# Kernel optimization log

Hardware: AMD Instinct MI355X
Metric: run time of the kernel (lower is better)

The kernel has to match this reference:

```python
import jax, jax.numpy as jnp
import numpy as np

B, L, D1, D2, N = 4, 2048, 1024, 1024, 4096

def setup_inputs() -> dict:
    key = jax.random.key(0)
    k1, k2, k3 = jax.random.split(key, 3)
    inputs = jax.random.normal(k1, (B, L, D1), dtype=jnp.float32)
    key_param_tokens = jax.random.normal(k2, (N, D1), dtype=jnp.float32) * 0.02
    value_param_tokens = jax.random.normal(k3, (N, D2), dtype=jnp.float32) * 0.02
    return {"inputs": inputs, "key_param_tokens": key_param_tokens, "value_param_tokens": value_param_tokens}

def reference(inputs, key_param_tokens, value_param_tokens):
    # scores: [B, L, N] = query @ key^T (scale_factor = 1, no mask, dropout_p = 0)
    attn_weight = jnp.einsum('bld,nd->bln', inputs, key_param_tokens)
    n = attn_weight.shape[-1]
    # 'l2_norm_gelu': L2-normalize over the param-token axis, rescale by sqrt(n), then exact GELU
    l2 = jnp.sqrt(jnp.sum(attn_weight * attn_weight, axis=-1, keepdims=True))
    normed = attn_weight / l2 * jnp.sqrt(jnp.asarray(n, attn_weight.dtype))
    attn_weight = jax.nn.gelu(normed, approximate=False)
    # output: [B, L, D2]
    return jnp.einsum('bln,nd->bld', attn_weight, value_param_tokens)
```

## Files before the change

kernel.cpp:

```cpp
#include <hip/hip_runtime.h>
#include <hip/hip_bf16.h>
#include <math.h>
#include <stdint.h>

typedef __attribute__((ext_vector_type(8))) short short8;
typedef __attribute__((ext_vector_type(4))) float f32x4;

__device__ inline short f2bf(float x) {
  union { float f; uint32_t u; } c; c.f = x;
  uint32_t r = (c.u + 0x7FFFu + ((c.u >> 16) & 1u)) >> 16;
  return (short)(uint16_t)r;
}
__device__ inline float bf2f(short s) {
  union { uint32_t u; float f; } c; c.u = ((uint32_t)(uint16_t)s) << 16;
  return c.f;
}

__device__ inline void gload16(const short* src, const char* ldsdst) {
  __builtin_amdgcn_global_load_lds(
      (const __attribute__((address_space(1))) void*)src,
      (__attribute__((address_space(3))) void*)ldsdst, 16, 0, 0);
}

#define BAR __builtin_amdgcn_s_barrier()
#define VMC(n) asm volatile("s_waitcnt vmcnt(" #n ")" ::: "memory")

__global__ void cvt2_kernel(const float* __restrict__ X, const float* __restrict__ Kp,
                            short* __restrict__ Xb, short* __restrict__ Kb,
                            int n8x, int n8tot) {
  int i = blockIdx.x * blockDim.x + threadIdx.x;
  if (i >= n8tot) return;
  const float* src = (i < n8x) ? X + (size_t)i * 8 : Kp + (size_t)(i - n8x) * 8;
  short* dst = (i < n8x) ? Xb + (size_t)i * 8 : Kb + (size_t)(i - n8x) * 8;
  const float4* p = (const float4*)src;
  float4 a = p[0], b = p[1];
  short8 o;
  o[0] = f2bf(a.x); o[1] = f2bf(a.y); o[2] = f2bf(a.z); o[3] = f2bf(a.w);
  o[4] = f2bf(b.x); o[5] = f2bf(b.y); o[6] = f2bf(b.z); o[7] = f2bf(b.w);
  *(short8*)dst = o;
}

__global__ void transpose_bf16_kernel(const float* __restrict__ V,
                                      short* __restrict__ Vt,
                                      int rows, int cols) {
  __shared__ float tile[64][65];
  int n0 = blockIdx.x * 64;
  int d0 = blockIdx.y * 64;
  int t = threadIdx.x;
#pragma unroll
  for (int r = 0; r < 16; ++r) {
    int idx = t + 256 * r;
    int rr = idx >> 6, cc = idx & 63;
    tile[rr][cc] = V[(size_t)(n0 + rr) * cols + d0 + cc];
  }
  __syncthreads();
#pragma unroll
  for (int r = 0; r < 16; ++r) {
    int idx = t + 256 * r;
    int dd = idx >> 6, nn = idx & 63;
    Vt[(size_t)(d0 + dd) * rows + n0 + nn] = f2bf(tile[nn][dd]);
  }
}

template <int N, int K, int BN, int WM, int WN, bool SCORE>
__global__ __launch_bounds__(512, 2) void gemm_ring(
    const short* __restrict__ A, const short* __restrict__ Bm,
    void* __restrict__ Cout, float* __restrict__ rowss) {
  constexpr int NT = K / 32;
  static_assert(NT % 3 == 2, "tail assumes NT%3==2");
  constexpr int ASZ = 256 * 32 * 2;
  constexpr int BSZ = BN * 32 * 2;
  constexpr int SLOT = ASZ + BSZ;
  constexpr int BR = BN / 128;
  constexpr int LQ = 2 + BR;
  constexpr int MH2 = 256 / WM / 32;
  constexpr int RW = 128 / WM;
  constexpr int NTN = N / BN;

  __shared__ char lds[3 * SLOT];

  const int t = threadIdx.x, lane = t & 63, w = t >> 6;
  const int wm = w / WN, wn = w % WN;
  const int idx = lane & 15, g = lane >> 4;

  const int bid = blockIdx.x;
  const int id2 = (bid & 7) * (4 * NTN) + (bid >> 3);
  const int row0 = (id2 / NTN) * 256, col0 = (id2 % NTN) * BN;

  const int sxor = ((t & 3) ^ ((t >> 2) & 3)) * 8;
  const short* gAp = A + (size_t)(row0 + (t >> 2)) * K + sxor;
  const short* gBp = Bm + (size_t)(col0 + (t >> 2)) * K + sxor;

  auto STG = [&](int s, int T) {
    const int kt = T * 32;
    char* base = (char*)lds + s * SLOT + t * 16;
#pragma unroll
    for (int r = 0; r < 2; ++r)
      gload16(gAp + (size_t)(r * 128) * K + kt, base + r * 8192);
#pragma unroll
    for (int r = 0; r < BR; ++r)
      gload16(gBp + (size_t)(r * 128) * K + kt, base + ASZ + r * 8192);
  };

  const int rdx = ((g ^ (idx & 3)) << 4);
  short8 a[2][MH2], b4[4];
  auto LD = [&](int s) {
    const char* base = (char*)lds + s * SLOT;
#pragma unroll
    for (int nf = 0; nf < 4; ++nf) {
      const int col = (BN == 256) ? (wn * 32 + (nf & 1) * 16 + (nf >> 1) * 128)
                                  : (wn * 64 + nf * 16);
      b4[nf] = *(const short8*)(base + ASZ + (col + idx) * 64 + rdx);
    }
#pragma unroll
    for (int mh = 0; mh < 2; ++mh)
#pragma unroll
      for (int f = 0; f < MH2; ++f) {
        const int row = mh * 128 + wm * RW + f * 16 + idx;
        a[mh][f] = *(const short8*)(base + row * 64 + rdx);
      }
  };

  f32x4 acc[2 * MH2][4] = {};
  auto MFM = [&]() {
    __builtin_amdgcn_s_setprio(1);
#pragma unroll
    for (int mh = 0; mh < 2; ++mh)
#pragma unroll
      for (int f = 0; f < MH2; ++f)
#pragma unroll
        for (int nf = 0; nf < 4; ++nf)
          acc[mh * MH2 + f][nf] = __builtin_amdgcn_mfma_f32_16x16x32_bf16(
              a[mh][f], b4[nf], acc[mh * MH2 + f][nf], 0, 0, 0);
    __builtin_amdgcn_s_setprio(0);
  };

  auto ITER = [&](int T, int s, int s2, bool mainL) {
    if (mainL) STG(s2, T + 2);
    LD(s);
    MFM();
    if (mainL) {
      if constexpr (LQ == 4) { VMC(4); } else { VMC(3); }
      BAR;
    } else if (T + 1 < NT) {
      VMC(0);
      BAR;
    }
  };

  STG(0, 0);
  STG(1, 1);
  if constexpr (LQ == 4) { VMC(4); } else { VMC(3); }
  BAR;

  for (int c = 0; c + 3 <= NT; c += 3) {
    ITER(c, 0, 2, true);
    ITER(c + 1, 1, 0, true);
    ITER(c + 2, 2, 1, true);
  }
  ITER(NT - 2, 0, 2, false);
  ITER(NT - 1, 1, 0, false);

  if constexpr (SCORE) {
    short* S = (short*)Cout;
#pragma unroll
    for (int mf = 0; mf < 2 * MH2; ++mf) {
#pragma unroll
      for (int j = 0; j < 4; ++j) {
        const int row = row0 + wm * RW + (mf % MH2) * 16 + (mf / MH2) * 128 + g * 4 + j;
        float ss = 0.f;
#pragma unroll
        for (int nf = 0; nf < 4; ++nf) {
          const float v = acc[mf][nf][j];
          ss += v * v;
          const int col = col0 + ((BN == 256)
                                      ? (wn * 32 + (nf & 1) * 16 + (nf >> 1) * 128)
                                      : (wn * 64 + nf * 16)) + idx;
          S[(size_t)row * N + col] = f2bf(v);
        }
        ss += __shfl_xor(ss, 1);
        ss += __shfl_xor(ss, 2);
        ss += __shfl_xor(ss, 4);
        ss += __shfl_xor(ss, 8);
        if (idx == 0) atomicAdd(&rowss[row], ss);
      }
    }
  } else {
    float* C = (float*)Cout;
#pragma unroll
    for (int mf = 0; mf < 2 * MH2; ++mf)
#pragma unroll
      for (int j = 0; j < 4; ++j) {
        const int row = row0 + wm * RW + (mf % MH2) * 16 + (mf / MH2) * 128 + g * 4 + j;
#pragma unroll
        for (int nf = 0; nf < 4; ++nf) {
          const int col = col0 + ((BN == 256)
                                      ? (wn * 32 + (nf & 1) * 16 + (nf >> 1) * 128)
                                      : (wn * 64 + nf * 16)) + idx;
          C[(size_t)row * N + col] = acc[mf][nf][j];
        }
      }
  }
}

__global__ void norm_gelu_kernel(short* __restrict__ S,
                                 const float* __restrict__ rowss, int total8) {
  int i = blockIdx.x * blockDim.x + threadIdx.x;
  if (i >= total8) return;
  size_t base = (size_t)i * 8;
  int row = (int)(base >> 12);
  float scale = 64.0f * rsqrtf(rowss[row]);
  short8 v = *(short8*)(S + base);
  short8 o;
#pragma unroll
  for (int k = 0; k < 8; ++k) {
    float x = bf2f(v[k]) * scale;
    float gl = 0.5f * x * (1.0f + erff(x * 0.70710678118654752f));
    o[k] = f2bf(gl);
  }
  *(short8*)(S + base) = o;
}

extern "C" void kernel_launch(void* const* d_in, const int* in_sizes, int n_in,
                              void* d_out, int out_size, void* d_ws,
                              size_t ws_size, hipStream_t stream) {
  const float* X = (const float*)d_in[0];
  const float* Kp = (const float*)d_in[1];
  const float* Vp = (const float*)d_in[2];
  float* out = (float*)d_out;

  const int M = 8192, D1 = 1024, Nn = 4096, D2 = 1024;

  char* ws = (char*)d_ws;
  short* Xb = (short*)ws; ws += (size_t)M * D1 * 2;
  short* Kb = (short*)ws; ws += (size_t)Nn * D1 * 2;
  short* Vt = (short*)ws; ws += (size_t)D2 * Nn * 2;
  short* S  = (short*)ws; ws += (size_t)M * Nn * 2;
  float* rowss = (float*)ws;
  (void)ws_size;

  hipMemsetAsync(rowss, 0, M * sizeof(float), stream);
  const int n8x = M * D1 / 8, n8k = Nn * D1 / 8;
  cvt2_kernel<<<(n8x + n8k + 255) / 256, 256, 0, stream>>>(X, Kp, Xb, Kb, n8x, n8x + n8k);
  transpose_bf16_kernel<<<dim3(Nn / 64, D2 / 64), 256, 0, stream>>>(Vp, Vt, Nn, D2);

  gemm_ring<4096, 1024, 256, 2, 4, true><<<512, 512, 0, stream>>>(Xb, Kb, S, rowss);
  norm_gelu_kernel<<<(M * Nn / 8 + 255) / 256, 256, 0, stream>>>(S, rowss, M * Nn / 8);
  gemm_ring<1024, 4096, 128, 4, 2, false><<<256, 512, 0, stream>>>(S, Vt, out, nullptr);
}
```

Baseline: 208.2 us.

## Overlap LDS fragment loads with MFMA via split half-iterations and double-buffered A

Restructures the GEMM main loop so each k-step is split into two MFMA halves. The barrier sits between them, and the A fragments for the next stage are loaded from LDS into a second register set while the second half computes. This hides LDS read latency behind matrix math. The LDS swizzle pattern is also changed to reduce bank conflicts, and the loop is unrolled by six to alternate register buffers. The extra A fragment registers may raise register pressure at 2 blocks per CU.

```diff
diff --git a/kernel.cpp b/kernel.cpp
--- a/kernel.cpp
+++ b/kernel.cpp
@@ -23,7 +23,7 @@
 }
 
 #define BAR __builtin_amdgcn_s_barrier()
-#define VMC(n) asm volatile("s_waitcnt vmcnt(" #n ")" ::: "memory")
+#define VMCL(n) asm volatile("s_waitcnt vmcnt(" #n ")" ::: "memory")
 
 __global__ void cvt2_kernel(const float* __restrict__ X, const float* __restrict__ Kp,
                             short* __restrict__ Xb, short* __restrict__ Kb,
@@ -63,17 +63,16 @@
 }
 
 template <int N, int K, int BN, int WM, int WN, bool SCORE>
-__global__ __launch_bounds__(512, 2) void gemm_ring(
+__global__ __launch_bounds__(512, 2) void gemm_ol(
     const short* __restrict__ A, const short* __restrict__ Bm,
     void* __restrict__ Cout, float* __restrict__ rowss) {
   constexpr int NT = K / 32;
-  static_assert(NT % 3 == 2, "tail assumes NT%3==2");
+  static_assert((NT - 2) % 6 == 0, "tail assumes NT%6==2");
   constexpr int ASZ = 256 * 32 * 2;
   constexpr int BSZ = BN * 32 * 2;
   constexpr int SLOT = ASZ + BSZ;
   constexpr int BR = BN / 128;
-  constexpr int LQ = 2 + BR;
-  constexpr int MH2 = 256 / WM / 32;
+  constexpr int MH2 = 128 / WM / 16;
   constexpr int RW = 128 / WM;
   constexpr int NTN = N / BN;
 
@@ -87,7 +86,7 @@
   const int id2 = (bid & 7) * (4 * NTN) + (bid >> 3);
   const int row0 = (id2 / NTN) * 256, col0 = (id2 % NTN) * BN;
 
-  const int sxor = ((t & 3) ^ ((t >> 2) & 3)) * 8;
+  const int sxor = ((t & 3) ^ ((t >> 3) & 3)) * 8;
   const short* gAp = A + (size_t)(row0 + (t >> 2)) * K + sxor;
   const short* gBp = Bm + (size_t)(col0 + (t >> 2)) * K + sxor;
 
@@ -102,64 +101,84 @@
       gload16(gBp + (size_t)(r * 128) * K + kt, base + ASZ + r * 8192);
   };
 
-  const int rdx = ((g ^ (idx & 3)) << 4);
-  short8 a[2][MH2], b4[4];
-  auto LD = [&](int s) {
-    const char* base = (char*)lds + s * SLOT;
-#pragma unroll
-    for (int nf = 0; nf < 4; ++nf) {
-      const int col = (BN == 256) ? (wn * 32 + (nf & 1) * 16 + (nf >> 1) * 128)
-                                  : (wn * 64 + nf * 16);
-      b4[nf] = *(const short8*)(base + ASZ + (col + idx) * 64 + rdx);
-    }
-#pragma unroll
-    for (int mh = 0; mh < 2; ++mh)
-#pragma unroll
-      for (int f = 0; f < MH2; ++f) {
-        const int row = mh * 128 + wm * RW + f * 16 + idx;
-        a[mh][f] = *(const short8*)(base + row * 64 + rdx);
-      }
-  };
-
+  const int rdx = (g ^ ((idx >> 1) & 3)) << 4;
+
+  short8 a0[2 * MH2], a1[2 * MH2], bfr[4];
   f32x4 acc[2 * MH2][4] = {};
-  auto MFM = [&]() {
-    __builtin_amdgcn_s_setprio(1);
-#pragma unroll
-    for (int mh = 0; mh < 2; ++mh)
-#pragma unroll
-      for (int f = 0; f < MH2; ++f)
-#pragma unroll
-        for (int nf = 0; nf < 4; ++nf)
-          acc[mh * MH2 + f][nf] = __builtin_amdgcn_mfma_f32_16x16x32_bf16(
-              a[mh][f], b4[nf], acc[mh * MH2 + f][nf], 0, 0, 0);
-    __builtin_amdgcn_s_setprio(0);
-  };
-
-  auto ITER = [&](int T, int s, int s2, bool mainL) {
-    if (mainL) STG(s2, T + 2);
-    LD(s);
-    MFM();
-    if (mainL) {
-      if constexpr (LQ == 4) { VMC(4); } else { VMC(3); }
-      BAR;
-    } else if (T + 1 < NT) {
-      VMC(0);
-      BAR;
-    }
-  };
+
+#define LDA_(S, ARR)                                                     \
+  {                                                                      \
+    const char* base_ = (char*)lds + (S)*SLOT;                           \
+    _Pragma("unroll") for (int mh = 0; mh < 2; ++mh)                     \
+        _Pragma("unroll") for (int f = 0; f < MH2; ++f) {                \
+      const int row_ = mh * 128 + wm * RW + f * 16 + idx;                \
+      ARR[mh * MH2 + f] = *(const short8*)(base_ + row_ * 64 + rdx);     \
+    }                                                                    \
+  }
+#define LDB_(S)                                                          \
+  {                                                                      \
+    const char* base_ = (char*)lds + (S)*SLOT + ASZ;                     \
+    _Pragma("unroll") for (int nf = 0; nf < 4; ++nf) {                   \
+      const int col_ = (BN == 256)                                       \
+                           ? (wn * 32 + (nf & 1) * 16 + (nf >> 1) * 128) \
+                           : (wn * 64 + nf * 16);                        \
+      bfr[nf] = *(const short8*)(base_ + (col_ + idx) * 64 + rdx);       \
+    }                                                                    \
+  }
+#define HALF_(MH, ARR)                                                   \
+  {                                                                      \
+    __builtin_amdgcn_s_setprio(1);                                       \
+    _Pragma("unroll") for (int f = 0; f < MH2; ++f)                      \
+        _Pragma("unroll") for (int nf = 0; nf < 4; ++nf)                 \
+            acc[(MH)*MH2 + f][nf] = __builtin_amdgcn_mfma_f32_16x16x32_bf16( \
+                ARR[(MH)*MH2 + f], bfr[nf], acc[(MH)*MH2 + f][nf], 0, 0, 0); \
+    __builtin_amdgcn_s_setprio(0);                                       \
+  }
+#define VMC_LQ                                  \
+  do {                                          \
+    if constexpr (BR == 2) { VMCL(4); } else { VMCL(3); } \
+  } while (0)
+#define ITER_(T, CUR, NXT, S, S1, S2) \
+  {                                   \
+    LDB_(S);                          \
+    STG(S2, (T) + 2);                 \
+    HALF_(0, CUR);                    \
+    VMC_LQ;                           \
+    BAR;                              \
+    LDA_(S1, NXT);                    \
+    HALF_(1, CUR);                    \
+  }
 
   STG(0, 0);
   STG(1, 1);
-  if constexpr (LQ == 4) { VMC(4); } else { VMC(3); }
+  VMC_LQ;
   BAR;
-
-  for (int c = 0; c + 3 <= NT; c += 3) {
-    ITER(c, 0, 2, true);
-    ITER(c + 1, 1, 0, true);
-    ITER(c + 2, 2, 1, true);
-  }
-  ITER(NT - 2, 0, 2, false);
-  ITER(NT - 1, 1, 0, false);
+  LDA_(0, a0);
+
+  for (int c = 0; c < NT - 2; c += 6) {
+    ITER_(c + 0, a0, a1, 0, 1, 2);
+    ITER_(c + 1, a1, a0, 1, 2, 0);
+    ITER_(c + 2, a0, a1, 2, 0, 1);
+    ITER_(c + 3, a1, a0, 0, 1, 2);
+    ITER_(c + 4, a0, a1, 1, 2, 0);
+    ITER_(c + 5, a1, a0, 2, 0, 1);
+  }
+  {
+    LDB_(0);
+    HALF_(0, a0);
+    VMCL(0);
+    BAR;
+    LDA_(1, a1);
+    HALF_(1, a0);
+    LDB_(1);
+    HALF_(0, a1);
+    HALF_(1, a1);
+  }
+#undef LDA_
+#undef LDB_
+#undef HALF_
+#undef VMC_LQ
+#undef ITER_
 
   if constexpr (SCORE) {
     short* S = (short*)Cout;
@@ -244,7 +263,7 @@
   cvt2_kernel<<<(n8x + n8k + 255) / 256, 256, 0, stream>>>(X, Kp, Xb, Kb, n8x, n8x + n8k);
   transpose_bf16_kernel<<<dim3(Nn / 64, D2 / 64), 256, 0, stream>>>(Vp, Vt, Nn, D2);
 
-  gemm_ring<4096, 1024, 256, 2, 4, true><<<512, 512, 0, stream>>>(Xb, Kb, S, rowss);
+  gemm_ol<4096, 1024, 256, 2, 4, true><<<512, 512, 0, stream>>>(Xb, Kb, S, rowss);
   norm_gelu_kernel<<<(M * Nn / 8 + 255) / 256, 256, 0, stream>>>(S, rowss, M * Nn / 8);
-  gemm_ring<1024, 4096, 128, 4, 2, false><<<256, 512, 0, stream>>>(S, Vt, out, nullptr);
-}
+  gemm_ol<1024, 4096, 128, 4, 2, false><<<256, 512, 0, stream>>>(S, Vt, out, nullptr);
+}
```

New measurement: 199.0 us. -4.4%, faster.

## Load B operand directly from global into registers, stage only A in LDS

Applied to the files above, without the earlier changes.

The GEMM kernels now stage only the A tile through LDS via a 3-slot ring. Each wave loads its B fragments straight from global memory into double-buffered registers one k-step ahead. The LDS swizzle is changed and the main loop is unrolled by six to alternate the register buffers. This cuts LDS footprint and LDS read traffic for B, but B reads become non-shared, uncoalesced per-wave global loads that rely on cache hits, and register pressure rises.

```diff
diff --git a/kernel.cpp b/kernel.cpp
--- a/kernel.cpp
+++ b/kernel.cpp
@@ -23,7 +23,9 @@
 }
 
 #define BAR __builtin_amdgcn_s_barrier()
-#define VMC(n) asm volatile("s_waitcnt vmcnt(" #n ")" ::: "memory")
+#define WAIT6 asm volatile("s_waitcnt vmcnt(6) lgkmcnt(0)" ::: "memory")
+#define WAIT4 asm volatile("s_waitcnt vmcnt(4) lgkmcnt(0)" ::: "memory")
+#define WAIT2 asm volatile("s_waitcnt vmcnt(2) lgkmcnt(0)" ::: "memory")
 
 __global__ void cvt2_kernel(const float* __restrict__ X, const float* __restrict__ Kp,
                             short* __restrict__ Xb, short* __restrict__ Kb,
@@ -63,21 +65,16 @@
 }
 
 template <int N, int K, int BN, int WM, int WN, bool SCORE>
-__global__ __launch_bounds__(512, 2) void gemm_ring(
+__global__ __launch_bounds__(512, 2) void gemm_hyb(
     const short* __restrict__ A, const short* __restrict__ Bm,
     void* __restrict__ Cout, float* __restrict__ rowss) {
   constexpr int NT = K / 32;
-  static_assert(NT % 3 == 2, "tail assumes NT%3==2");
+  static_assert((NT - 2) % 6 == 0, "unroll-6 tail assumes NT%6==2");
   constexpr int ASZ = 256 * 32 * 2;
-  constexpr int BSZ = BN * 32 * 2;
-  constexpr int SLOT = ASZ + BSZ;
-  constexpr int BR = BN / 128;
-  constexpr int LQ = 2 + BR;
-  constexpr int MH2 = 256 / WM / 32;
-  constexpr int RW = 128 / WM;
+  constexpr int MF = 256 / WM / 16;
   constexpr int NTN = N / BN;
 
-  __shared__ char lds[3 * SLOT];
+  __shared__ char lds[3 * ASZ];
 
   const int t = threadIdx.x, lane = t & 63, w = t >> 6;
   const int wm = w / WN, wn = w % WN;
@@ -87,96 +84,97 @@
   const int id2 = (bid & 7) * (4 * NTN) + (bid >> 3);
   const int row0 = (id2 / NTN) * 256, col0 = (id2 % NTN) * BN;
 
-  const int sxor = ((t & 3) ^ ((t >> 2) & 3)) * 8;
+  const int sxor = ((t & 3) ^ ((t >> 3) & 3)) * 8;
   const short* gAp = A + (size_t)(row0 + (t >> 2)) * K + sxor;
-  const short* gBp = Bm + (size_t)(col0 + (t >> 2)) * K + sxor;
 
   auto STG = [&](int s, int T) {
     const int kt = T * 32;
-    char* base = (char*)lds + s * SLOT + t * 16;
+    char* base = (char*)lds + s * ASZ + t * 16;
 #pragma unroll
     for (int r = 0; r < 2; ++r)
       gload16(gAp + (size_t)(r * 128) * K + kt, base + r * 8192);
-#pragma unroll
-    for (int r = 0; r < BR; ++r)
-      gload16(gBp + (size_t)(r * 128) * K + kt, base + ASZ + r * 8192);
-  };
-
-  const int rdx = ((g ^ (idx & 3)) << 4);
-  short8 a[2][MH2], b4[4];
-  auto LD = [&](int s) {
-    const char* base = (char*)lds + s * SLOT;
-#pragma unroll
-    for (int nf = 0; nf < 4; ++nf) {
-      const int col = (BN == 256) ? (wn * 32 + (nf & 1) * 16 + (nf >> 1) * 128)
-                                  : (wn * 64 + nf * 16);
-      b4[nf] = *(const short8*)(base + ASZ + (col + idx) * 64 + rdx);
+  };
+
+  const int rdx = (g ^ ((idx >> 1) & 3)) << 4;
+  short8 a[MF], b0[4], b1[4];
+
+  auto LDA = [&](int s) {
+    const char* base = (char*)lds + s * ASZ;
+#pragma unroll
+    for (int f = 0; f < MF; ++f) {
+      const int row = wm * (256 / WM) + f * 16 + idx;
+      a[f] = *(const short8*)(base + row * 64 + rdx);
     }
-#pragma unroll
-    for (int mh = 0; mh < 2; ++mh)
-#pragma unroll
-      for (int f = 0; f < MH2; ++f) {
-        const int row = mh * 128 + wm * RW + f * 16 + idx;
-        a[mh][f] = *(const short8*)(base + row * 64 + rdx);
-      }
-  };
-
-  f32x4 acc[2 * MH2][4] = {};
-  auto MFM = [&]() {
+  };
+
+  const short* gBp = Bm + (size_t)(col0 + wn * 64 + idx) * K + g * 8;
+  auto GLB = [&](int T, short8(&bb)[4]) {
+    const int kt = T * 32;
+#pragma unroll
+    for (int nf = 0; nf < 4; ++nf)
+      bb[nf] = *(const short8*)(gBp + (size_t)(nf * 16) * K + kt);
+  };
+
+  f32x4 acc[MF][4] = {};
+  auto MFM = [&](short8(&bb)[4]) {
     __builtin_amdgcn_s_setprio(1);
 #pragma unroll
-    for (int mh = 0; mh < 2; ++mh)
-#pragma unroll
-      for (int f = 0; f < MH2; ++f)
-#pragma unroll
-        for (int nf = 0; nf < 4; ++nf)
-          acc[mh * MH2 + f][nf] = __builtin_amdgcn_mfma_f32_16x16x32_bf16(
-              a[mh][f], b4[nf], acc[mh * MH2 + f][nf], 0, 0, 0);
+    for (int f = 0; f < MF; ++f)
+#pragma unroll
+      for (int nf = 0; nf < 4; ++nf)
+        acc[f][nf] = __builtin_amdgcn_mfma_f32_16x16x32_bf16(
+            a[f], bb[nf], acc[f][nf], 0, 0, 0);
     __builtin_amdgcn_s_setprio(0);
   };
 
-  auto ITER = [&](int T, int s, int s2, bool mainL) {
-    if (mainL) STG(s2, T + 2);
-    LD(s);
-    MFM();
-    if (mainL) {
-      if constexpr (LQ == 4) { VMC(4); } else { VMC(3); }
-      BAR;
-    } else if (T + 1 < NT) {
-      VMC(0);
-      BAR;
-    }
-  };
+#define BODY(T, S, S2, BC, BN_)  \
+  {                              \
+    STG(S2, (T) + 2);            \
+    GLB((T) + 1, BN_);           \
+    LDA(S);                      \
+    MFM(BC);                     \
+    WAIT6;                       \
+    BAR;                         \
+  }
 
   STG(0, 0);
   STG(1, 1);
-  if constexpr (LQ == 4) { VMC(4); } else { VMC(3); }
+  GLB(0, b0);
+  WAIT2;
   BAR;
 
-  for (int c = 0; c + 3 <= NT; c += 3) {
-    ITER(c, 0, 2, true);
-    ITER(c + 1, 1, 0, true);
-    ITER(c + 2, 2, 1, true);
-  }
-  ITER(NT - 2, 0, 2, false);
-  ITER(NT - 1, 1, 0, false);
+  for (int c = 0; c < NT - 2; c += 6) {
+    BODY(c + 0, 0, 2, b0, b1);
+    BODY(c + 1, 1, 0, b1, b0);
+    BODY(c + 2, 2, 1, b0, b1);
+    BODY(c + 3, 0, 2, b1, b0);
+    BODY(c + 4, 1, 0, b0, b1);
+    BODY(c + 5, 2, 1, b1, b0);
+  }
+  {
+    GLB(NT - 1, b1);
+    LDA(0);
+    MFM(b0);
+    WAIT4;
+    BAR;
+    LDA(1);
+    MFM(b1);
+  }
+#undef BODY
 
   if constexpr (SCORE) {
     short* S = (short*)Cout;
 #pragma unroll
-    for (int mf = 0; mf < 2 * MH2; ++mf) {
+    for (int mf = 0; mf < MF; ++mf) {
 #pragma unroll
       for (int j = 0; j < 4; ++j) {
-        const int row = row0 + wm * RW + (mf % MH2) * 16 + (mf / MH2) * 128 + g * 4 + j;
+        const int row = row0 + wm * (256 / WM) + mf * 16 + g * 4 + j;
         float ss = 0.f;
 #pragma unroll
         for (int nf = 0; nf < 4; ++nf) {
           const float v = acc[mf][nf][j];
           ss += v * v;
-          const int col = col0 + ((BN == 256)
-                                      ? (wn * 32 + (nf & 1) * 16 + (nf >> 1) * 128)
-                                      : (wn * 64 + nf * 16)) + idx;
-          S[(size_t)row * N + col] = f2bf(v);
+          S[(size_t)row * N + col0 + wn * 64 + nf * 16 + idx] = f2bf(v);
         }
         ss += __shfl_xor(ss, 1);
         ss += __shfl_xor(ss, 2);
@@ -188,17 +186,13 @@
   } else {
     float* C = (float*)Cout;
 #pragma unroll
-    for (int mf = 0; mf < 2 * MH2; ++mf)
+    for (int mf = 0; mf < MF; ++mf)
 #pragma unroll
       for (int j = 0; j < 4; ++j) {
-        const int row = row0 + wm * RW + (mf % MH2) * 16 + (mf / MH2) * 128 + g * 4 + j;
-#pragma unroll
-        for (int nf = 0; nf < 4; ++nf) {
-          const int col = col0 + ((BN == 256)
-                                      ? (wn * 32 + (nf & 1) * 16 + (nf >> 1) * 128)
-                                      : (wn * 64 + nf * 16)) + idx;
-          C[(size_t)row * N + col] = acc[mf][nf][j];
-        }
+        const int row = row0 + wm * (256 / WM) + mf * 16 + g * 4 + j;
+#pragma unroll
+        for (int nf = 0; nf < 4; ++nf)
+          C[(size_t)row * N + col0 + wn * 64 + nf * 16 + idx] = acc[mf][nf][j];
       }
   }
 }
@@ -244,7 +238,7 @@
   cvt2_kernel<<<(n8x + n8k + 255) / 256, 256, 0, stream>>>(X, Kp, Xb, Kb, n8x, n8x + n8k);
   transpose_bf16_kernel<<<dim3(Nn / 64, D2 / 64), 256, 0, stream>>>(Vp, Vt, Nn, D2);
 
-  gemm_ring<4096, 1024, 256, 2, 4, true><<<512, 512, 0, stream>>>(Xb, Kb, S, rowss);
+  gemm_hyb<4096, 1024, 256, 2, 4, true><<<512, 512, 0, stream>>>(Xb, Kb, S, rowss);
   norm_gelu_kernel<<<(M * Nn / 8 + 255) / 256, 256, 0, stream>>>(S, rowss, M * Nn / 8);
-  gemm_ring<1024, 4096, 128, 4, 2, false><<<256, 512, 0, stream>>>(S, Vt, out, nullptr);
-}
+  gemm_hyb<1024, 4096, 128, 4, 2, false><<<256, 512, 0, stream>>>(S, Vt, out, nullptr);
+}
```

Result: slower. 325.1 us (+56.1%).
